# Kernel optimization log

Measured on AMD Instinct MI355X. Metric: run time of the kernel, lower is better.

## Reference

```python
import jax, jax.numpy as jnp
import numpy as np

EMBED_DIM = 768
NUM_HEADS = 12
HEAD_DIM = EMBED_DIM // NUM_HEADS


def setup_inputs() -> dict:
    key = jax.random.key(0)
    ks = jax.random.split(key, 9)
    B, S, E = 8, 1024, EMBED_DIM
    scale = 1.0 / np.sqrt(E)
    inputs = jax.random.normal(ks[0], (B, S, E), dtype=jnp.float32)
    Wq = jax.random.normal(ks[1], (E, E), dtype=jnp.float32) * scale
    Wk = jax.random.normal(ks[2], (E, E), dtype=jnp.float32) * scale
    Wv = jax.random.normal(ks[3], (E, E), dtype=jnp.float32) * scale
    Wo = jax.random.normal(ks[4], (E, E), dtype=jnp.float32) * scale
    bq = jnp.zeros((E,), dtype=jnp.float32)
    bk = jnp.zeros((E,), dtype=jnp.float32)
    bv = jnp.zeros((E,), dtype=jnp.float32)
    bo = jnp.zeros((E,), dtype=jnp.float32)
    return {"inputs": inputs, "Wq": Wq, "bq": bq, "Wk": Wk, "bk": bk,
            "Wv": Wv, "bv": bv, "Wo": Wo, "bo": bo}


def reference(inputs, Wq, bq, Wk, bk, Wv, bv, Wo, bo):
    B, S, E = inputs.shape
    H, D = NUM_HEADS, HEAD_DIM

    def split_heads(x):  # [B,S,E] -> [B,H,S,D]
        return x.reshape(B, S, H, D).transpose(0, 2, 1, 3)

    q = split_heads(inputs @ Wq + bq)
    k = split_heads(inputs @ Wk + bk)
    v = split_heads(inputs @ Wv + bv)

    # scaled dot-product attention; note: scale uses sqrt(last dim of key) = sqrt(D)
    score = jnp.einsum('bhqd,bhkd->bhqk', q, k) / jnp.sqrt(jnp.float32(D))
    weights = jax.nn.softmax(score, axis=-1)
    attn = jnp.einsum('bhqk,bhkd->bhqd', weights, v)  # [B,H,S,D]

    concat = attn.transpose(0, 2, 1, 3).reshape(B, S, E)
    return concat @ Wo + bo
```

## Files before the change

kernel.cpp:

```cpp
#include <hip/hip_runtime.h>
#include <hip/hip_bf16.h>
#include <cstddef>

#define E_DIM  768
#define S_LEN  1024
#define NHEADS 12
#define HDIM   64
#define BATCH  8
#define TOKENS (BATCH * S_LEN)
#define WELEMS (E_DIM * E_DIM)

typedef short bf16x8 __attribute__((ext_vector_type(8)));
typedef short bf16x4 __attribute__((ext_vector_type(4)));
typedef float f32x4  __attribute__((ext_vector_type(4)));

#define MFMA16(a, b, c)   __builtin_amdgcn_mfma_f32_16x16x32_bf16((a), (b), (c), 0, 0, 0)
#define MFMA16K16(a, b, c) __builtin_amdgcn_mfma_f32_16x16x16bf16_1k((a), (b), (c), 0, 0, 0)

#define GLD_LDS16(gp, lp)                                                  \
    __builtin_amdgcn_global_load_lds(                                      \
        (const __attribute__((address_space(1))) void*)(gp),               \
        (__attribute__((address_space(3))) void*)(lp), 16, 0, 0)

#define QSCALE 0.180336880f

static __device__ __forceinline__ short f2bf(float f) {
    union { float f; unsigned int u; } cv; cv.f = f;
    unsigned int u = cv.u + 0x7fffu + ((cv.u >> 16) & 1u);
    return (short)(u >> 16);
}

__global__ __launch_bounds__(256) void xcvt_kernel(
    const float* __restrict__ X, short* __restrict__ Y)
{
    const size_t i = ((size_t)blockIdx.x * 256 + threadIdx.x) * 8;
    const float4 a = *(const float4*)&X[i];
    const float4 b = *(const float4*)&X[i + 4];
    bf16x8 o;
    o[0] = f2bf(a.x); o[1] = f2bf(a.y); o[2] = f2bf(a.z); o[3] = f2bf(a.w);
    o[4] = f2bf(b.x); o[5] = f2bf(b.y); o[6] = f2bf(b.z); o[7] = f2bf(b.w);
    *(bf16x8*)&Y[i] = o;
}

__global__ __launch_bounds__(256) void transpose_w(
    const float* __restrict__ s0, const float* __restrict__ s1,
    const float* __restrict__ s2, const float* __restrict__ s3,
    short* __restrict__ dst)
{
    const int z = blockIdx.z;
    const float* S = (z == 0) ? s0 : (z == 1) ? s1 : (z == 2) ? s2 : s3;
    short* D = dst + (size_t)z * WELEMS;
    __shared__ float t[64][65];
    const int r = threadIdx.x >> 2, c0 = (threadIdx.x & 3) * 16;
    const int br = blockIdx.x * 64, bc = blockIdx.y * 64;
    #pragma unroll
    for (int j = 0; j < 4; ++j) {
        float4 v = *(const float4*)&S[(size_t)(br + r) * E_DIM + bc + c0 + j * 4];
        t[r][c0 + j * 4 + 0] = v.x; t[r][c0 + j * 4 + 1] = v.y;
        t[r][c0 + j * 4 + 2] = v.z; t[r][c0 + j * 4 + 3] = v.w;
    }
    __syncthreads();
    #pragma unroll
    for (int half = 0; half < 2; ++half) {
        bf16x8 o;
        #pragma unroll
        for (int j = 0; j < 8; ++j) o[j] = f2bf(t[c0 + half * 8 + j][r]);
        *(bf16x8*)&D[(size_t)(bc + r) * E_DIM + br + c0 + half * 8] = o;
    }
}

template<bool AF32>
__global__ __launch_bounds__(256, 3) void gemm_qkv_t(
    const void* __restrict__ Ap, const short* __restrict__ Wt,
    const float* __restrict__ bq, const float* __restrict__ bk,
    const float* __restrict__ bv, short* __restrict__ oq,
    short* __restrict__ ok, short* __restrict__ ov)
{
    __shared__ __align__(16) short As[128 * 64];
    __shared__ __align__(16) short Bs[128 * 64];

    const int tid  = threadIdx.x;
    const int wave = tid >> 6, lane = tid & 63;
    const int quad = lane >> 4, l16 = lane & 15;
    const int bm = blockIdx.x * 128;
    const int by = blockIdx.y;
    const int wsel = by / 6;
    const int nb = (by % 6) * 128;
    const short* wt = Wt + (size_t)wsel * WELEMS;
    const float* bias = (wsel == 0) ? bq : (wsel == 1) ? bk : bv;
    short* outp = (wsel == 0) ? oq : (wsel == 1) ? ok : ov;
    const int wm = (wave >> 1) * 64, wn = (wave & 1) * 64;

    f32x4 acc[4][4];
    #pragma unroll
    for (int mt = 0; mt < 4; ++mt)
        #pragma unroll
        for (int nt = 0; nt < 4; ++nt) acc[mt][nt] = (f32x4){0.f, 0.f, 0.f, 0.f};

    for (int k0 = 0; k0 < E_DIM; k0 += 64) {
        if (AF32) {
            const float* A = (const float*)Ap;
            float4 ax[4][2];
            #pragma unroll
            for (int i = 0; i < 4; ++i) {
                const int slot = i * 256 + tid;
                const int row = slot >> 3, cl = slot & 7;
                const float4* gp = (const float4*)&A[(size_t)(bm + row) * E_DIM + k0 + cl * 8];
                ax[i][0] = gp[0]; ax[i][1] = gp[1];
            }
            __syncthreads();
            #pragma unroll
            for (int i = 0; i < 4; ++i) {
                const int slot = i * 256 + tid;
                const int row = slot >> 3, cl = slot & 7, cg = cl ^ (row & 7);
                GLD_LDS16(&wt[(size_t)(nb + row) * E_DIM + k0 + cg * 8], &Bs[slot * 8]);
            }
            #pragma unroll
            for (int i = 0; i < 4; ++i) {
                const int slot = i * 256 + tid;
                const int row = slot >> 3, cl = slot & 7, cs = cl ^ (row & 7);
                bf16x8 v8;
                v8[0] = f2bf(ax[i][0].x); v8[1] = f2bf(ax[i][0].y);
                v8[2] = f2bf(ax[i][0].z); v8[3] = f2bf(ax[i][0].w);
                v8[4] = f2bf(ax[i][1].x); v8[5] = f2bf(ax[i][1].y);
                v8[6] = f2bf(ax[i][1].z); v8[7] = f2bf(ax[i][1].w);
                *(bf16x8*)&As[row * 64 + cs * 8] = v8;
            }
        } else {
            const short* A = (const short*)Ap;
            __syncthreads();
            #pragma unroll
            for (int i = 0; i < 4; ++i) {
                const int slot = i * 256 + tid;
                const int row = slot >> 3, cl = slot & 7, cg = cl ^ (row & 7);
                GLD_LDS16(&A[(size_t)(bm + row) * E_DIM + k0 + cg * 8], &As[slot * 8]);
            }
            #pragma unroll
            for (int i = 0; i < 4; ++i) {
                const int slot = i * 256 + tid;
                const int row = slot >> 3, cl = slot & 7, cg = cl ^ (row & 7);
                GLD_LDS16(&wt[(size_t)(nb + row) * E_DIM + k0 + cg * 8], &Bs[slot * 8]);
            }
        }
        __syncthreads();

        #pragma unroll
        for (int ks = 0; ks < 2; ++ks) {
            bf16x8 a[4], b[4];
            #pragma unroll
            for (int mt = 0; mt < 4; ++mt) {
                const int row = wm + mt * 16 + l16;
                const int c = (ks * 4 + quad) ^ (row & 7);
                a[mt] = *(const bf16x8*)&As[row * 64 + c * 8];
            }
            #pragma unroll
            for (int nt = 0; nt < 4; ++nt) {
                const int row = wn + nt * 16 + l16;
                const int c = (ks * 4 + quad) ^ (row & 7);
                b[nt] = *(const bf16x8*)&Bs[row * 64 + c * 8];
            }
            #pragma unroll
            for (int mt = 0; mt < 4; ++mt)
                #pragma unroll
                for (int nt = 0; nt < 4; ++nt)
                    acc[mt][nt] = MFMA16(a[mt], b[nt], acc[mt][nt]);
        }
    }

    const float qscale = (wsel == 0) ? QSCALE : 1.0f;
    #pragma unroll
    for (int nt = 0; nt < 4; ++nt) {
        const int ncol = nb + wn + nt * 16 + l16;
        const float bvv = bias[ncol];
        const int h = ncol >> 6, d = ncol & (HDIM - 1);
        #pragma unroll
        for (int mt = 0; mt < 4; ++mt) {
            const int grow = bm + wm + mt * 16 + quad * 4;
            if (wsel < 2) {
                #pragma unroll
                for (int r = 0; r < 4; ++r) {
                    const int g = grow + r, b = g >> 10, s = g & (S_LEN - 1);
                    outp[((size_t)(b * NHEADS + h) * S_LEN + s) * HDIM + d] =
                        f2bf((acc[mt][nt][r] + bvv) * qscale);
                }
            } else {
                const int b = grow >> 10, s0 = grow & (S_LEN - 1);
                bf16x4 pv;
                #pragma unroll
                for (int r = 0; r < 4; ++r) pv[r] = f2bf(acc[mt][nt][r] + bvv);
                *(bf16x4*)&outp[((size_t)(b * NHEADS + h) * HDIM + d) * S_LEN + s0] = pv;
            }
        }
    }
}

__global__ __launch_bounds__(256, 3) void gemm_out_kernel(
    const short* __restrict__ A, const short* __restrict__ Wt,
    const float* __restrict__ bias, float* __restrict__ out)
{
    __shared__ __align__(16) short As[128 * 64];
    __shared__ __align__(16) short Bs[128 * 64];

    const int tid  = threadIdx.x;
    const int wave = tid >> 6, lane = tid & 63;
    const int quad = lane >> 4, l16 = lane & 15;
    const int bm = blockIdx.x * 128, nb = blockIdx.y * 128;
    const int wm = (wave >> 1) * 64, wn = (wave & 1) * 64;

    f32x4 acc[4][4];
    #pragma unroll
    for (int mt = 0; mt < 4; ++mt)
        #pragma unroll
        for (int nt = 0; nt < 4; ++nt) acc[mt][nt] = (f32x4){0.f, 0.f, 0.f, 0.f};

    for (int k0 = 0; k0 < E_DIM; k0 += 64) {
        __syncthreads();
        #pragma unroll
        for (int i = 0; i < 4; ++i) {
            const int slot = i * 256 + tid;
            const int row = slot >> 3, cl = slot & 7, cg = cl ^ (row & 7);
            GLD_LDS16(&A[(size_t)(bm + row) * E_DIM + k0 + cg * 8], &As[slot * 8]);
        }
        #pragma unroll
        for (int i = 0; i < 4; ++i) {
            const int slot = i * 256 + tid;
            const int row = slot >> 3, cl = slot & 7, cg = cl ^ (row & 7);
            GLD_LDS16(&Wt[(size_t)(nb + row) * E_DIM + k0 + cg * 8], &Bs[slot * 8]);
        }
        __syncthreads();

        #pragma unroll
        for (int ks = 0; ks < 2; ++ks) {
            bf16x8 a[4], b[4];
            #pragma unroll
            for (int mt = 0; mt < 4; ++mt) {
                const int row = wm + mt * 16 + l16;
                const int c = (ks * 4 + quad) ^ (row & 7);
                a[mt] = *(const bf16x8*)&As[row * 64 + c * 8];
            }
            #pragma unroll
            for (int nt = 0; nt < 4; ++nt) {
                const int row = wn + nt * 16 + l16;
                const int c = (ks * 4 + quad) ^ (row & 7);
                b[nt] = *(const bf16x8*)&Bs[row * 64 + c * 8];
            }
            #pragma unroll
            for (int mt = 0; mt < 4; ++mt)
                #pragma unroll
                for (int nt = 0; nt < 4; ++nt)
                    acc[mt][nt] = MFMA16(a[mt], b[nt], acc[mt][nt]);
        }
    }

    #pragma unroll
    for (int nt = 0; nt < 4; ++nt) {
        const int ncol = nb + wn + nt * 16 + l16;
        const float bvv = bias[ncol];
        #pragma unroll
        for (int mt = 0; mt < 4; ++mt) {
            const int grow = bm + wm + mt * 16 + quad * 4;
            #pragma unroll
            for (int r = 0; r < 4; ++r)
                out[(size_t)(grow + r) * E_DIM + ncol] = acc[mt][nt][r] + bvv;
        }
    }
}

__global__ __launch_bounds__(256) void attn_kernel(
    const short* __restrict__ Q, const short* __restrict__ K,
    const short* __restrict__ V, short* __restrict__ O)
{
    __shared__ __align__(16) short Ks[2][64 * 64];
    __shared__ __align__(16) short Vt[2][64 * 64];

    const int tid  = threadIdx.x;
    const int wave = tid >> 6, lane = tid & 63;
    const int quad = lane >> 4, l16 = lane & 15;
    const int bh = blockIdx.x;
    const int q0 = blockIdx.y * 128;
    const size_t base = (size_t)bh * S_LEN * HDIM;
    const short* Qb = Q + base;
    const short* Kb = K + base;
    const short* Vb = V + base;

    bf16x8 qa[2][2];
    #pragma unroll
    for (int mt = 0; mt < 2; ++mt)
        #pragma unroll
        for (int ks = 0; ks < 2; ++ks)
            qa[mt][ks] = *(const bf16x8*)&Qb[
                (size_t)(q0 + wave * 32 + mt * 16 + l16) * HDIM + ks * 32 + quad * 8];

    bf16x4 ones4;
    #pragma unroll
    for (int j = 0; j < 4; ++j) ones4[j] = (short)0x3F80;

    f32x4 oacc[2][4], lacc[2];
    #pragma unroll
    for (int mt = 0; mt < 2; ++mt) {
        #pragma unroll
        for (int nt = 0; nt < 4; ++nt) oacc[mt][nt] = (f32x4){0.f, 0.f, 0.f, 0.f};
        lacc[mt] = (f32x4){0.f, 0.f, 0.f, 0.f};
    }

    #pragma unroll
    for (int i = 0; i < 2; ++i) {
        const int slot = i * 256 + tid;
        const int row = slot >> 3, cl = slot & 7, cg = cl ^ (row & 7);
        GLD_LDS16(&Kb[(size_t)row * HDIM + cg * 8], &Ks[0][slot * 8]);
        GLD_LDS16(&Vb[(size_t)row * S_LEN + cg * 8], &Vt[0][slot * 8]);
    }

    for (int it = 0; it < S_LEN / 64; ++it) {
        __syncthreads();
        if (it + 1 < S_LEN / 64) {
            const int kt = (it + 1) * 64, nb = (it + 1) & 1;
            #pragma unroll
            for (int i = 0; i < 2; ++i) {
                const int slot = i * 256 + tid;
                const int row = slot >> 3, cl = slot & 7, cg = cl ^ (row & 7);
                GLD_LDS16(&Kb[(size_t)(kt + row) * HDIM + cg * 8], &Ks[nb][slot * 8]);
                GLD_LDS16(&Vb[(size_t)row * S_LEN + kt + cg * 8], &Vt[nb][slot * 8]);
            }
        }
        const short* ksb = Ks[it & 1];
        const short* vtb = Vt[it & 1];

        f32x4 sc[2][4];
        #pragma unroll
        for (int mt = 0; mt < 2; ++mt)
            #pragma unroll
            for (int t = 0; t < 4; ++t) sc[mt][t] = (f32x4){0.f, 0.f, 0.f, 0.f};
        #pragma unroll
        for (int ks = 0; ks < 2; ++ks)
            #pragma unroll
            for (int t = 0; t < 4; ++t) {
                const int row = t * 16 + l16;
                const int c = (ks * 4 + quad) ^ (row & 7);
                const bf16x8 kf = *(const bf16x8*)&ksb[row * 64 + c * 8];
                #pragma unroll
                for (int mt = 0; mt < 2; ++mt)
                    sc[mt][t] = MFMA16(kf, qa[mt][ks], sc[mt][t]);
            }

        bf16x4 pa16[2][4];
        #pragma unroll
        for (int mt = 0; mt < 2; ++mt)
            #pragma unroll
            for (int t = 0; t < 4; ++t)
                #pragma unroll
                for (int r = 0; r < 4; ++r)
                    pa16[mt][t][r] = f2bf(__builtin_amdgcn_exp2f(sc[mt][t][r]));

        #pragma unroll
        for (int t = 0; t < 4; ++t) {
            #pragma unroll
            for (int mt = 0; mt < 2; ++mt)
                lacc[mt] = MFMA16K16(pa16[mt][t], ones4, lacc[mt]);
            #pragma unroll
            for (int nt = 0; nt < 4; ++nt) {
                const int row = nt * 16 + l16;
                const int c = (t * 2 + (quad >> 1)) ^ (row & 7);
                const bf16x4 vb = *(const bf16x4*)&vtb[row * 64 + c * 8 + (quad & 1) * 4];
                #pragma unroll
                for (int mt = 0; mt < 2; ++mt)
                    oacc[mt][nt] = MFMA16K16(pa16[mt][t], vb, oacc[mt][nt]);
            }
        }
    }

    const int b = bh / NHEADS, h = bh - b * NHEADS;
    #pragma unroll
    for (int mt = 0; mt < 2; ++mt)
        #pragma unroll
        for (int nt = 0; nt < 4; ++nt)
            #pragma unroll
            for (int r = 0; r < 4; ++r) {
                const int qrow = q0 + wave * 32 + mt * 16 + quad * 4 + r;
                const float val = oacc[mt][nt][r] / lacc[mt][r];
                O[(size_t)(b * S_LEN + qrow) * E_DIM + h * HDIM + nt * 16 + l16] = f2bf(val);
            }
}

extern "C" void kernel_launch(void* const* d_in, const int* in_sizes, int n_in,
                              void* d_out, int out_size, void* d_ws, size_t ws_size,
                              hipStream_t stream) {
    const float* X  = (const float*)d_in[0];
    const float* Wq = (const float*)d_in[1];
    const float* bq = (const float*)d_in[2];
    const float* Wk = (const float*)d_in[3];
    const float* bk = (const float*)d_in[4];
    const float* Wv = (const float*)d_in[5];
    const float* bv = (const float*)d_in[6];
    const float* Wo = (const float*)d_in[7];
    const float* bo = (const float*)d_in[8];
    float* out = (float*)d_out;

    const size_t t = (size_t)TOKENS * E_DIM;
    short* q    = (short*)d_ws;
    short* k    = q + t;
    short* vT   = k + t;
    short* attn = vT + t;

    const size_t fast_need = (5 * t + 4 * (size_t)WELEMS) * 2;
    if (ws_size >= fast_need) {
        short* wt4 = attn + t;
        short* xbf = wt4 + 4 * (size_t)WELEMS;
        xcvt_kernel<<<(TOKENS * E_DIM / 8) / 256, 256, 0, stream>>>(X, xbf);
        transpose_w<<<dim3(12, 12, 4), 256, 0, stream>>>(Wq, Wk, Wv, Wo, wt4);
        gemm_qkv_t<false><<<dim3(TOKENS / 128, 18), 256, 0, stream>>>(
            xbf, wt4, bq, bk, bv, q, k, vT);
        attn_kernel<<<dim3(BATCH * NHEADS, S_LEN / 128), 256, 0, stream>>>(q, k, vT, attn);
        gemm_out_kernel<<<dim3(TOKENS / 128, 6), 256, 0, stream>>>(
            attn, wt4 + 3 * (size_t)WELEMS, bo, out);
    } else {
        short* wt_qkv = attn;
        short* wt_o   = q;
        transpose_w<<<dim3(12, 12, 3), 256, 0, stream>>>(Wq, Wk, Wv, Wv, wt_qkv);
        gemm_qkv_t<true><<<dim3(TOKENS / 128, 18), 256, 0, stream>>>(
            X, wt_qkv, bq, bk, bv, q, k, vT);
        attn_kernel<<<dim3(BATCH * NHEADS, S_LEN / 128), 256, 0, stream>>>(q, k, vT, attn);
        transpose_w<<<dim3(12, 12, 1), 256, 0, stream>>>(Wo, Wo, Wo, Wo, wt_o);
        gemm_out_kernel<<<dim3(TOKENS / 128, 6), 256, 0, stream>>>(attn, wt_o, bo, out);
    }
}
```

Measured before the change: 201.5 us.

## Pack bf16 conversions, remap GEMM blocks per XCD, store Q transposed

Replaces the per-element bf16 conversion with a packed two-at-a-time conversion using a byte permute, applied across all kernels. It rounds half-up instead of round-to-nearest-even. The QKV and output GEMMs switch to a 1D grid with an XCD-aware block remap, so blocks sharing weight or activation tiles land on the same L2. Q is now written transposed like V, with the softmax scale folded in, and attention gathers Q with strided scalar loads; this makes Q stores vectorized at the cost of an uncoalesced Q load in attention.

```diff
diff --git a/kernel.cpp b/kernel.cpp
--- a/kernel.cpp
+++ b/kernel.cpp
@@ -30,16 +30,27 @@
     return (short)(u >> 16);
 }
 
+static __device__ __forceinline__ unsigned int pk2(float f0, float f1) {
+    union { float f; unsigned int u; } a, b;
+    a.f = f0; b.f = f1;
+    return __builtin_amdgcn_perm(b.u + 0x8000u, a.u + 0x8000u, 0x07060302u);
+}
+static __device__ __forceinline__ bf16x4 pk4(float f0, float f1, float f2, float f3) {
+    union { unsigned int u[2]; bf16x4 v; } r;
+    r.u[0] = pk2(f0, f1); r.u[1] = pk2(f2, f3);
+    return r.v;
+}
+
 __global__ __launch_bounds__(256) void xcvt_kernel(
     const float* __restrict__ X, short* __restrict__ Y)
 {
     const size_t i = ((size_t)blockIdx.x * 256 + threadIdx.x) * 8;
     const float4 a = *(const float4*)&X[i];
     const float4 b = *(const float4*)&X[i + 4];
-    bf16x8 o;
-    o[0] = f2bf(a.x); o[1] = f2bf(a.y); o[2] = f2bf(a.z); o[3] = f2bf(a.w);
-    o[4] = f2bf(b.x); o[5] = f2bf(b.y); o[6] = f2bf(b.z); o[7] = f2bf(b.w);
-    *(bf16x8*)&Y[i] = o;
+    union { unsigned int u[4]; bf16x8 v; } o;
+    o.u[0] = pk2(a.x, a.y); o.u[1] = pk2(a.z, a.w);
+    o.u[2] = pk2(b.x, b.y); o.u[3] = pk2(b.z, b.w);
+    *(bf16x8*)&Y[i] = o.v;
 }
 
 __global__ __launch_bounds__(256) void transpose_w(
@@ -62,10 +73,13 @@
     __syncthreads();
     #pragma unroll
     for (int half = 0; half < 2; ++half) {
-        bf16x8 o;
-        #pragma unroll
-        for (int j = 0; j < 8; ++j) o[j] = f2bf(t[c0 + half * 8 + j][r]);
-        *(bf16x8*)&D[(size_t)(bc + r) * E_DIM + br + c0 + half * 8] = o;
+        union { unsigned int u[2]; bf16x4 v; } o0, o1;
+        o0.u[0] = pk2(t[c0 + half * 8 + 0][r], t[c0 + half * 8 + 1][r]);
+        o0.u[1] = pk2(t[c0 + half * 8 + 2][r], t[c0 + half * 8 + 3][r]);
+        o1.u[0] = pk2(t[c0 + half * 8 + 4][r], t[c0 + half * 8 + 5][r]);
+        o1.u[1] = pk2(t[c0 + half * 8 + 6][r], t[c0 + half * 8 + 7][r]);
+        *(bf16x4*)&D[(size_t)(bc + r) * E_DIM + br + c0 + half * 8]     = o0.v;
+        *(bf16x4*)&D[(size_t)(bc + r) * E_DIM + br + c0 + half * 8 + 4] = o1.v;
     }
 }
 
@@ -82,10 +96,12 @@
     const int tid  = threadIdx.x;
     const int wave = tid >> 6, lane = tid & 63;
     const int quad = lane >> 4, l16 = lane & 15;
-    const int bm = blockIdx.x * 128;
-    const int by = blockIdx.y;
-    const int wsel = by / 6;
-    const int nb = (by % 6) * 128;
+    const int bid = blockIdx.x;
+    const int xcd = bid & 7, qq = bid >> 3;
+    const int nblk = qq >> 3;
+    const int bm = (xcd * 8 + (qq & 7)) * 128;
+    const int wsel = nblk / 6;
+    const int nb = (nblk % 6) * 128;
     const short* wt = Wt + (size_t)wsel * WELEMS;
     const float* bias = (wsel == 0) ? bq : (wsel == 1) ? bk : bv;
     short* outp = (wsel == 0) ? oq : (wsel == 1) ? ok : ov;
@@ -119,12 +135,12 @@
             for (int i = 0; i < 4; ++i) {
                 const int slot = i * 256 + tid;
                 const int row = slot >> 3, cl = slot & 7, cs = cl ^ (row & 7);
-                bf16x8 v8;
-                v8[0] = f2bf(ax[i][0].x); v8[1] = f2bf(ax[i][0].y);
-                v8[2] = f2bf(ax[i][0].z); v8[3] = f2bf(ax[i][0].w);
-                v8[4] = f2bf(ax[i][1].x); v8[5] = f2bf(ax[i][1].y);
-                v8[6] = f2bf(ax[i][1].z); v8[7] = f2bf(ax[i][1].w);
-                *(bf16x8*)&As[row * 64 + cs * 8] = v8;
+                union { unsigned int u[4]; bf16x8 v; } v8;
+                v8.u[0] = pk2(ax[i][0].x, ax[i][0].y);
+                v8.u[1] = pk2(ax[i][0].z, ax[i][0].w);
+                v8.u[2] = pk2(ax[i][1].x, ax[i][1].y);
+                v8.u[3] = pk2(ax[i][1].z, ax[i][1].w);
+                *(bf16x8*)&As[row * 64 + cs * 8] = v8.v;
             }
         } else {
             const short* A = (const short*)Ap;
@@ -176,18 +192,19 @@
         #pragma unroll
         for (int mt = 0; mt < 4; ++mt) {
             const int grow = bm + wm + mt * 16 + quad * 4;
-            if (wsel < 2) {
+            if (wsel == 1) {
                 #pragma unroll
                 for (int r = 0; r < 4; ++r) {
                     const int g = grow + r, b = g >> 10, s = g & (S_LEN - 1);
                     outp[((size_t)(b * NHEADS + h) * S_LEN + s) * HDIM + d] =
-                        f2bf((acc[mt][nt][r] + bvv) * qscale);
+                        f2bf(acc[mt][nt][r] + bvv);
                 }
             } else {
                 const int b = grow >> 10, s0 = grow & (S_LEN - 1);
-                bf16x4 pv;
-                #pragma unroll
-                for (int r = 0; r < 4; ++r) pv[r] = f2bf(acc[mt][nt][r] + bvv);
+                bf16x4 pv = pk4((acc[mt][nt][0] + bvv) * qscale,
+                                (acc[mt][nt][1] + bvv) * qscale,
+                                (acc[mt][nt][2] + bvv) * qscale,
+                                (acc[mt][nt][3] + bvv) * qscale);
                 *(bf16x4*)&outp[((size_t)(b * NHEADS + h) * HDIM + d) * S_LEN + s0] = pv;
             }
         }
@@ -204,7 +221,10 @@
     const int tid  = threadIdx.x;
     const int wave = tid >> 6, lane = tid & 63;
     const int quad = lane >> 4, l16 = lane & 15;
-    const int bm = blockIdx.x * 128, nb = blockIdx.y * 128;
+    const int bid = blockIdx.x;
+    const int xcd = bid & 7, qq = bid >> 3;
+    const int nb = (qq >> 3) * 128;
+    const int bm = (xcd * 8 + (qq & 7)) * 128;
     const int wm = (wave >> 1) * 64, wn = (wave & 1) * 64;
 
     f32x4 acc[4][4];
@@ -287,9 +307,12 @@
     #pragma unroll
     for (int mt = 0; mt < 2; ++mt)
         #pragma unroll
-        for (int ks = 0; ks < 2; ++ks)
-            qa[mt][ks] = *(const bf16x8*)&Qb[
-                (size_t)(q0 + wave * 32 + mt * 16 + l16) * HDIM + ks * 32 + quad * 8];
+        for (int ks = 0; ks < 2; ++ks) {
+            const int s = q0 + wave * 32 + mt * 16 + l16;
+            #pragma unroll
+            for (int j = 0; j < 8; ++j)
+                qa[mt][ks][j] = Qb[(size_t)(ks * 32 + quad * 8 + j) * S_LEN + s];
+        }
 
     bf16x4 ones4;
     #pragma unroll
@@ -314,13 +337,13 @@
     for (int it = 0; it < S_LEN / 64; ++it) {
         __syncthreads();
         if (it + 1 < S_LEN / 64) {
-            const int kt = (it + 1) * 64, nb = (it + 1) & 1;
+            const int kt = (it + 1) * 64, nbf = (it + 1) & 1;
             #pragma unroll
             for (int i = 0; i < 2; ++i) {
                 const int slot = i * 256 + tid;
                 const int row = slot >> 3, cl = slot & 7, cg = cl ^ (row & 7);
-                GLD_LDS16(&Kb[(size_t)(kt + row) * HDIM + cg * 8], &Ks[nb][slot * 8]);
-                GLD_LDS16(&Vb[(size_t)row * S_LEN + kt + cg * 8], &Vt[nb][slot * 8]);
+                GLD_LDS16(&Kb[(size_t)(kt + row) * HDIM + cg * 8], &Ks[nbf][slot * 8]);
+                GLD_LDS16(&Vb[(size_t)row * S_LEN + kt + cg * 8], &Vt[nbf][slot * 8]);
             }
         }
         const short* ksb = Ks[it & 1];
@@ -348,9 +371,10 @@
         for (int mt = 0; mt < 2; ++mt)
             #pragma unroll
             for (int t = 0; t < 4; ++t)
-                #pragma unroll
-                for (int r = 0; r < 4; ++r)
-                    pa16[mt][t][r] = f2bf(__builtin_amdgcn_exp2f(sc[mt][t][r]));
+                pa16[mt][t] = pk4(__builtin_amdgcn_exp2f(sc[mt][t][0]),
+                                  __builtin_amdgcn_exp2f(sc[mt][t][1]),
+                                  __builtin_amdgcn_exp2f(sc[mt][t][2]),
+                                  __builtin_amdgcn_exp2f(sc[mt][t][3]));
 
         #pragma unroll
         for (int t = 0; t < 4; ++t) {
@@ -408,19 +432,19 @@
         short* xbf = wt4 + 4 * (size_t)WELEMS;
         xcvt_kernel<<<(TOKENS * E_DIM / 8) / 256, 256, 0, stream>>>(X, xbf);
         transpose_w<<<dim3(12, 12, 4), 256, 0, stream>>>(Wq, Wk, Wv, Wo, wt4);
-        gemm_qkv_t<false><<<dim3(TOKENS / 128, 18), 256, 0, stream>>>(
+        gemm_qkv_t<false><<<1152, 256, 0, stream>>>(
             xbf, wt4, bq, bk, bv, q, k, vT);
         attn_kernel<<<dim3(BATCH * NHEADS, S_LEN / 128), 256, 0, stream>>>(q, k, vT, attn);
-        gemm_out_kernel<<<dim3(TOKENS / 128, 6), 256, 0, stream>>>(
+        gemm_out_kernel<<<384, 256, 0, stream>>>(
             attn, wt4 + 3 * (size_t)WELEMS, bo, out);
     } else {
         short* wt_qkv = attn;
         short* wt_o   = q;
         transpose_w<<<dim3(12, 12, 3), 256, 0, stream>>>(Wq, Wk, Wv, Wv, wt_qkv);
-        gemm_qkv_t<true><<<dim3(TOKENS / 128, 18), 256, 0, stream>>>(
+        gemm_qkv_t<true><<<1152, 256, 0, stream>>>(
             X, wt_qkv, bq, bk, bv, q, k, vT);
         attn_kernel<<<dim3(BATCH * NHEADS, S_LEN / 128), 256, 0, stream>>>(q, k, vT, attn);
         transpose_w<<<dim3(12, 12, 1), 256, 0, stream>>>(Wo, Wo, Wo, Wo, wt_o);
-        gemm_out_kernel<<<dim3(TOKENS / 128, 6), 256, 0, stream>>>(attn, wt_o, bo, out);
-    }
-}
+        gemm_out_kernel<<<384, 256, 0, stream>>>(attn, wt_o, bo, out);
+    }
+}
```

After: 191.6 us. -4.9%, faster.
